# Optimization experiments

Hardware: AMD Instinct MI355X
Metric: run time of the kernel (lower is better)

The kernel has to match this reference:

```python
import jax, jax.numpy as jnp
import numpy as np

EMB = 768
HEADS = 8
HEAD_DIM = EMB // HEADS
SCALE = HEAD_DIM ** -0.5


def setup_inputs() -> dict:
    key = jax.random.key(0)
    ks = jax.random.split(key, 9)
    s = 0.02
    return {
        "x": jax.random.normal(ks[0], (2, 4096, EMB), dtype=jnp.float32),
        "Wq": jax.random.normal(ks[1], (EMB, EMB), dtype=jnp.float32) * s,
        "bq": jax.random.normal(ks[2], (EMB,), dtype=jnp.float32) * s,
        "Wk": jax.random.normal(ks[3], (EMB, EMB), dtype=jnp.float32) * s,
        "bk": jax.random.normal(ks[4], (EMB,), dtype=jnp.float32) * s,
        "Wv": jax.random.normal(ks[5], (EMB, EMB), dtype=jnp.float32) * s,
        "bv": jax.random.normal(ks[6], (EMB,), dtype=jnp.float32) * s,
        "Wo": jax.random.normal(ks[7], (EMB, EMB), dtype=jnp.float32) * s,
        "bo": jax.random.normal(ks[8], (EMB,), dtype=jnp.float32) * s,
    }


def reference(x, Wq, bq, Wk, bk, Wv, bv, Wo, bo):
    b, n, _ = x.shape
    # torch Linear: y = x @ W.T + b
    def split_heads(y):  # [b, n, emb] -> [b, h, n, d]
        return y.reshape(b, n, HEADS, HEAD_DIM).transpose(0, 2, 1, 3)

    q = split_heads(x @ Wq.T + bq)
    k = split_heads(x @ Wk.T + bk)
    v = split_heads(x @ Wv.T + bv)
    # scores [b, h, q, k]; source applies scaling inside softmax input
    scores = jnp.einsum('bhqd,bhkd->bhqk', q, k) * SCALE
    weight = jax.nn.softmax(scores, axis=-1)
    out = jnp.einsum('bhqk,bhkd->bhqd', weight, v)
    out = out.transpose(0, 2, 1, 3).reshape(b, n, EMB)
    return out @ Wo.T + bo
```

## Files before the change

kernel.cpp:

```cpp
#include <hip/hip_runtime.h>


typedef __bf16 bf16;
typedef __attribute__((ext_vector_type(4))) float f32x4;
typedef __attribute__((ext_vector_type(16))) float f32x16;
typedef __attribute__((ext_vector_type(8))) __bf16 bf16x8;
typedef __attribute__((ext_vector_type(4))) __bf16 bf16x4;
typedef __attribute__((ext_vector_type(4))) unsigned u32x4;

#define EMB 768
#define SEQ 4096
#define NB 2
#define NHEADS 8
#define HD 96
#define BHTOT (NB * NHEADS)
#define MTOT (NB * SEQ)
#define QSCALE 0.14724241052735512f

#define AS1 __attribute__((address_space(1)))
#define AS3 __attribute__((address_space(3)))

__global__ __launch_bounds__(256) void cast_f32_bf16(const float* __restrict__ in,
                                                     bf16* __restrict__ out) {
  const int i = (blockIdx.x * 256 + threadIdx.x) * 4;
  const f32x4 v = *reinterpret_cast<const f32x4*>(in + i);
  bf16x4 o;
  o[0] = (bf16)v[0]; o[1] = (bf16)v[1]; o[2] = (bf16)v[2]; o[3] = (bf16)v[3];
  *reinterpret_cast<bf16x4*>(out + i) = o;
}

__global__ __launch_bounds__(256) void cast_w4(const float* __restrict__ w0,
                                               const float* __restrict__ w1,
                                               const float* __restrict__ w2,
                                               const float* __restrict__ w3,
                                               bf16* __restrict__ o0,
                                               bf16* __restrict__ o1,
                                               bf16* __restrict__ o2,
                                               bf16* __restrict__ o3) {
  const float* w = (blockIdx.y == 0) ? w0 : (blockIdx.y == 1) ? w1 : (blockIdx.y == 2) ? w2 : w3;
  bf16* o = (blockIdx.y == 0) ? o0 : (blockIdx.y == 1) ? o1 : (blockIdx.y == 2) ? o2 : o3;
  const int i = (blockIdx.x * 256 + threadIdx.x) * 4;
  const f32x4 v = *reinterpret_cast<const f32x4*>(w + i);
  bf16x4 ob;
  ob[0] = (bf16)v[0]; ob[1] = (bf16)v[1]; ob[2] = (bf16)v[2]; ob[3] = (bf16)v[3];
  *reinterpret_cast<bf16x4*>(o + i) = ob;
}

template <int MODE>
__global__ __launch_bounds__(256) void gemm_bt(const bf16* __restrict__ A,
                                               const bf16* __restrict__ B,
                                               const float* __restrict__ b0,
                                               const float* __restrict__ b1,
                                               const float* __restrict__ b2,
                                               void* __restrict__ out,
                                               void* __restrict__ outK) {
  constexpr int K = EMB;
  __shared__ bf16 As[128 * 32];
  __shared__ bf16 Bs[128 * 32];
  const int tid = threadIdx.x;
  const int lane = tid & 63;
  const int wid = tid >> 6;
  const int wr = wid >> 1, wc = wid & 1;
  const int l15 = lane & 15, l4 = lane >> 4;
  const int rowBase = blockIdx.y * 128;
  const int colBase = blockIdx.x * 128;

  f32x4 acc[4][4] = {};

  for (int kt = 0; kt < K / 32; ++kt) {
    const int kb = kt * 32;
#pragma unroll
    for (int i = 0; i < 2; ++i) {
      const int c = (wid * 2 + i) * 64 + lane;
      const int row = c >> 2, cc = c & 3;
      const bf16* ga = A + (size_t)(rowBase + row) * K + kb + cc * 8;
      const bf16* gb = B + (size_t)(colBase + row) * K + kb + cc * 8;
      __builtin_amdgcn_global_load_lds(
          (const AS1 void*)ga,
          (AS3 void*)(As + (size_t)(wid * 2 + i) * 512), 16, 0, 0);
      __builtin_amdgcn_global_load_lds(
          (const AS1 void*)gb,
          (AS3 void*)(Bs + (size_t)(wid * 2 + i) * 512), 16, 0, 0);
    }
    __syncthreads();
    bf16x8 af[4], bfr[4];
#pragma unroll
    for (int t = 0; t < 4; ++t) {
      af[t]  = *reinterpret_cast<const bf16x8*>(As + (wr * 64 + t * 16 + l15) * 32 + l4 * 8);
      bfr[t] = *reinterpret_cast<const bf16x8*>(Bs + (wc * 64 + t * 16 + l15) * 32 + l4 * 8);
    }
#pragma unroll
    for (int mt = 0; mt < 4; ++mt)
#pragma unroll
      for (int nt = 0; nt < 4; ++nt)
        acc[mt][nt] = __builtin_amdgcn_mfma_f32_16x16x32_bf16(af[mt], bfr[nt], acc[mt][nt], 0, 0, 0);
    __syncthreads();
  }

#pragma unroll
  for (int mt = 0; mt < 4; ++mt) {
#pragma unroll
    for (int nt = 0; nt < 4; ++nt) {
      const int gn = colBase + wc * 64 + nt * 16 + l15;
      if (MODE == 0) {
        const int mm = gn / 768;
        const int g7 = gn - mm * 768;
        const int h = g7 / HD, d = g7 - h * HD;
        const float* bp = (mm == 0) ? b0 : (mm == 1) ? b1 : b2;
        const float bv = bp[g7];
        const float sc = (mm == 0) ? QSCALE : 1.f;
#pragma unroll
        for (int r = 0; r < 4; ++r) {
          const int gm = rowBase + wr * 64 + mt * 16 + l4 * 4 + r;
          const int b = gm >> 12, n = gm & (SEQ - 1);
          const float v = (acc[mt][nt][r] + bv) * sc;
          if (mm == 1) {
            ((bf16*)outK)[((size_t)(b * NHEADS + h) * SEQ + n) * 128 +
                          (((d >> 3) ^ (n & 7)) << 3) + (d & 7)] = (bf16)v;
          } else {
            bf16* dst = (bf16*)out + (mm == 2 ? (size_t)MTOT * EMB : 0);
            dst[((size_t)(b * NHEADS + h) * SEQ + n) * HD + d] = (bf16)v;
          }
        }
      } else {
        const float bv = b0[gn];
#pragma unroll
        for (int r = 0; r < 4; ++r) {
          const int gm = rowBase + wr * 64 + mt * 16 + l4 * 4 + r;
          ((float*)out)[(size_t)gm * EMB + gn] = acc[mt][nt][r] + bv;
        }
      }
    }
  }
}

__global__ __launch_bounds__(256) void transpose_v(const bf16* __restrict__ v,
                                                   bf16* __restrict__ vt) {
  __shared__ bf16 T[96][72];
  const int bh = blockIdx.y;
  const int n0 = blockIdx.x * 64;
  const int tid = threadIdx.x;
#pragma unroll
  for (int i = 0; i < 3; ++i) {
    const int c = i * 256 + tid;
    const int n = c / 12, cc = c % 12;
    const bf16x8 val = *reinterpret_cast<const bf16x8*>(
        v + ((size_t)bh * SEQ + n0 + n) * HD + cc * 8);
#pragma unroll
    for (int j = 0; j < 8; ++j) T[cc * 8 + j][n] = val[j];
  }
  __syncthreads();
#pragma unroll
  for (int i = 0; i < 3; ++i) {
    const int c = i * 256 + tid;
    const int d = c >> 3, nc = c & 7;
    const int s0i = (nc >> 1) * 16 + (nc & 1) * 4;
    const bf16x4 lo = *reinterpret_cast<const bf16x4*>(&T[d][s0i]);
    const bf16x4 hi = *reinterpret_cast<const bf16x4*>(&T[d][s0i + 8]);
    const bf16x8 val = __builtin_shufflevector(lo, hi, 0, 1, 2, 3, 4, 5, 6, 7);
    const int pc = nc ^ (d & 7);
    *reinterpret_cast<bf16x8*>(vt + ((size_t)bh * HD + d) * SEQ + n0 + pc * 8) = val;
  }
}

__global__ __launch_bounds__(256) void attn_fwd(const bf16* __restrict__ q,
                                                const bf16* __restrict__ ksw,
                                                const bf16* __restrict__ vt,
                                                bf16* __restrict__ o) {
  __shared__ bf16 Ks[2][64 * 128];
  __shared__ bf16 Vts[2][96 * 64];
  const int tid = threadIdx.x;
  const int lane = tid & 63;
  const int wid = tid >> 6;
  const int l31 = lane & 31, lhi = lane >> 5;
  const int lin = blockIdx.y * 16 + blockIdx.x;
  const int l2 = (lin & 7) * 32 + (lin >> 3);
  const int qblk = l2 & 15, bh = l2 >> 4;
  const int q0 = qblk * 256 + wid * 64;
  const size_t headq = (size_t)bh * SEQ * HD;
  const bf16* kg = ksw + (size_t)bh * SEQ * 128;
  const bf16* vg = vt + (size_t)bh * (size_t)HD * SEQ;

  const bf16* kp = kg + (size_t)tid * 8;
  const bf16* vp = vg + (size_t)(tid >> 3) * SEQ + (tid & 7) * 8;

  int krd[12], vrd[12];
#pragma unroll
  for (int kib = 0; kib < 2; ++kib)
#pragma unroll
    for (int dc = 0; dc < 6; ++dc) {
      const int row = kib * 32 + l31;
      krd[kib * 6 + dc] = (row * 128 + (((dc * 2 + lhi) ^ (l31 & 7)) * 8)) * 2;
    }
#pragma unroll
  for (int db = 0; db < 3; ++db)
#pragma unroll
    for (int kb = 0; kb < 4; ++kb) {
      const int row = db * 32 + l31;
      vrd[db * 4 + kb] = (row * 64 + (((kb * 2 + lhi) ^ (l31 & 7)) * 8)) * 2;
    }

  bf16x8 qf[2][6];
#pragma unroll
  for (int g = 0; g < 2; ++g)
#pragma unroll
    for (int dc = 0; dc < 6; ++dc)
      qf[g][dc] = *reinterpret_cast<const bf16x8*>(
          q + headq + (size_t)(q0 + g * 32 + l31) * HD + dc * 16 + lhi * 8);

  f32x16 oacc[2][3] = {};
  float lrun[2] = {0.f, 0.f};

#pragma unroll
  for (int i = 0; i < 4; ++i)
    __builtin_amdgcn_global_load_lds((const AS1 void*)(kp + i * 2048),
                                     (AS3 void*)(&Ks[0][i * 2048 + wid * 512]), 16, 0, 0);
#pragma unroll
  for (int i = 0; i < 3; ++i)
    __builtin_amdgcn_global_load_lds((const AS1 void*)(vp + (size_t)i * 131072),
                                     (AS3 void*)(&Vts[0][i * 2048 + wid * 512]), 16, 0, 0);
  kp += 8192;
  vp += 64;
  __syncthreads();

  constexpr int NT = SEQ / 64;
  for (int kt = 0; kt < NT; ++kt) {
    const int cur = kt & 1;
    if (kt < NT - 1) {
#pragma unroll
      for (int i = 0; i < 4; ++i)
        __builtin_amdgcn_global_load_lds((const AS1 void*)(kp + i * 2048),
                                         (AS3 void*)(&Ks[cur ^ 1][i * 2048 + wid * 512]), 16, 0, 0);
#pragma unroll
      for (int i = 0; i < 3; ++i)
        __builtin_amdgcn_global_load_lds((const AS1 void*)(vp + (size_t)i * 131072),
                                         (AS3 void*)(&Vts[cur ^ 1][i * 2048 + wid * 512]), 16, 0, 0);
      kp += 8192;
      vp += 64;
    }
    const char* ksb = (const char*)Ks[cur];
    const char* vsb = (const char*)Vts[cur];

    bf16x8 pf[2][4];
#pragma unroll
    for (int kib = 0; kib < 2; ++kib) {
      f32x16 s[2] = {};
      __builtin_amdgcn_s_setprio(1);
#pragma unroll
      for (int dc = 0; dc < 6; ++dc) {
        const bf16x8 kf = *reinterpret_cast<const bf16x8*>(ksb + krd[kib * 6 + dc]);
        s[0] = __builtin_amdgcn_mfma_f32_32x32x16_bf16(kf, qf[0][dc], s[0], 0, 0, 0);
        s[1] = __builtin_amdgcn_mfma_f32_32x32x16_bf16(kf, qf[1][dc], s[1], 0, 0, 0);
      }
      __builtin_amdgcn_s_setprio(0);
#pragma unroll
      for (int g = 0; g < 2; ++g) {
        float a0 = 0.f, a1 = 0.f, a2 = 0.f, a3 = 0.f;
#pragma unroll
        for (int i = 0; i < 4; ++i) {
          s[g][4 * i + 0] = __builtin_amdgcn_exp2f(s[g][4 * i + 0]); a0 += s[g][4 * i + 0];
          s[g][4 * i + 1] = __builtin_amdgcn_exp2f(s[g][4 * i + 1]); a1 += s[g][4 * i + 1];
          s[g][4 * i + 2] = __builtin_amdgcn_exp2f(s[g][4 * i + 2]); a2 += s[g][4 * i + 2];
          s[g][4 * i + 3] = __builtin_amdgcn_exp2f(s[g][4 * i + 3]); a3 += s[g][4 * i + 3];
        }
        lrun[g] += (a0 + a1) + (a2 + a3);
        unsigned c[8];
#pragma unroll
        for (int i = 0; i < 8; ++i)
          asm("v_cvt_pk_bf16_f32 %0, %1, %2"
              : "=v"(c[i]) : "v"(s[g][2 * i]), "v"(s[g][2 * i + 1]));
        const u32x4 wa = {c[0], c[1], c[2], c[3]};
        const u32x4 wb = {c[4], c[5], c[6], c[7]};
        pf[g][kib * 2 + 0] = __builtin_bit_cast(bf16x8, wa);
        pf[g][kib * 2 + 1] = __builtin_bit_cast(bf16x8, wb);
      }
    }

    __builtin_amdgcn_s_setprio(1);
#pragma unroll
    for (int kb = 0; kb < 4; ++kb) {
#pragma unroll
      for (int db = 0; db < 3; ++db) {
        const bf16x8 vf = *reinterpret_cast<const bf16x8*>(vsb + vrd[db * 4 + kb]);
        oacc[0][db] = __builtin_amdgcn_mfma_f32_32x32x16_bf16(vf, pf[0][kb], oacc[0][db], 0, 0, 0);
        oacc[1][db] = __builtin_amdgcn_mfma_f32_32x32x16_bf16(vf, pf[1][kb], oacc[1][db], 0, 0, 0);
      }
    }
    __builtin_amdgcn_s_setprio(0);

    __syncthreads();
  }

  const int b = bh >> 3, h = bh & 7;
#pragma unroll
  for (int g = 0; g < 2; ++g) {
    float lr = lrun[g];
    lr += __shfl_xor(lr, 32, 64);
    const float inv = 1.f / lr;
    const int n = q0 + g * 32 + l31;
    bf16* obase = o + (size_t)(b * SEQ + n) * EMB + h * HD;
#pragma unroll
    for (int db = 0; db < 3; ++db) {
#pragma unroll
      for (int i = 0; i < 8; ++i) {
        const int r = 2 * i;
        const int d = db * 32 + (r & 3) + 8 * (r >> 2) + 4 * lhi;
        unsigned w;
        const float v0 = oacc[g][db][r] * inv, v1 = oacc[g][db][r + 1] * inv;
        asm("v_cvt_pk_bf16_f32 %0, %1, %2" : "=v"(w) : "v"(v0), "v"(v1));
        *reinterpret_cast<unsigned*>(obase + d) = w;
      }
    }
  }
}

extern "C" void kernel_launch(void* const* d_in, const int* in_sizes, int n_in,
                              void* d_out, int out_size, void* d_ws, size_t ws_size,
                              hipStream_t stream) {
  const float* x  = (const float*)d_in[0];
  const float* Wq = (const float*)d_in[1];
  const float* bq = (const float*)d_in[2];
  const float* Wk = (const float*)d_in[3];
  const float* bk = (const float*)d_in[4];
  const float* Wv = (const float*)d_in[5];
  const float* bv = (const float*)d_in[6];
  const float* Wo = (const float*)d_in[7];
  const float* bo = (const float*)d_in[8];

  const size_t XN = (size_t)MTOT * EMB;
  const size_t WN = (size_t)EMB * EMB;
  const size_t KSWN = (size_t)BHTOT * SEQ * 128;

  bf16* p = (bf16*)d_ws;
  bf16* xbf  = p; p += XN;
  bf16* wqb  = p; p += WN;
  bf16* wkb  = p; p += WN;
  bf16* wvb  = p; p += WN;
  bf16* wob  = p; p += WN;
  bf16* qb   = p; p += XN;
  bf16* vb   = p; p += XN;
  bf16* kbsw = p; p += KSWN;
  bf16* vtb  = p; p += XN;
  bf16* ao   = p; p += XN;

  cast_f32_bf16<<<XN / 1024, 256, 0, stream>>>(x, xbf);
  cast_w4<<<dim3(WN / 1024, 4), 256, 0, stream>>>(Wq, Wk, Wv, Wo, wqb, wkb, wvb, wob);

  gemm_bt<0><<<dim3(3 * EMB / 128, MTOT / 128), 256, 0, stream>>>(
      xbf, wqb, bq, bk, bv, qb, kbsw);

  transpose_v<<<dim3(SEQ / 64, BHTOT), 256, 0, stream>>>(vb, vtb);

  attn_fwd<<<dim3(SEQ / 256, BHTOT), 256, 0, stream>>>(qb, kbsw, vtb, ao);

  gemm_bt<1><<<dim3(EMB / 128, MTOT / 128), 256, 0, stream>>>(
      ao, wob, bo, nullptr, nullptr, d_out, nullptr);
}
```

Before: 237.3 us.

## Split attention KV range in two with fp32 partials and a merge kernel

```diff
diff --git a/kernel.cpp b/kernel.cpp
--- a/kernel.cpp
+++ b/kernel.cpp
@@ -2,6 +2,7 @@
 
 
 typedef __bf16 bf16;
+typedef __attribute__((ext_vector_type(2))) float f32x2;
 typedef __attribute__((ext_vector_type(4))) float f32x4;
 typedef __attribute__((ext_vector_type(16))) float f32x16;
 typedef __attribute__((ext_vector_type(8))) __bf16 bf16x8;
@@ -163,26 +164,34 @@
   }
 }
 
-__global__ __launch_bounds__(256) void attn_fwd(const bf16* __restrict__ q,
-                                                const bf16* __restrict__ ksw,
-                                                const bf16* __restrict__ vt,
-                                                bf16* __restrict__ o) {
+template <int SPLIT>
+__global__ __launch_bounds__(256, 2) void attn_fwd(const bf16* __restrict__ q,
+                                                   const bf16* __restrict__ ksw,
+                                                   const bf16* __restrict__ vt,
+                                                   void* __restrict__ outp,
+                                                   float* __restrict__ lsum) {
   __shared__ bf16 Ks[2][64 * 128];
   __shared__ bf16 Vts[2][96 * 64];
   const int tid = threadIdx.x;
   const int lane = tid & 63;
   const int wid = tid >> 6;
   const int l31 = lane & 31, lhi = lane >> 5;
-  const int lin = blockIdx.y * 16 + blockIdx.x;
-  const int l2 = (lin & 7) * 32 + (lin >> 3);
-  const int qblk = l2 & 15, bh = l2 >> 4;
+  const int lin = (blockIdx.z * gridDim.y + blockIdx.y) * gridDim.x + blockIdx.x;
+  const int nblk = 256 * SPLIT;
+  const int cpx = nblk >> 3;
+  const int l2 = (lin & 7) * cpx + (lin >> 3);
+  const int qblk = l2 & 15;
+  const int z = (SPLIT == 2) ? ((l2 >> 4) & 1) : 0;
+  const int bh = (SPLIT == 2) ? (l2 >> 5) : (l2 >> 4);
   const int q0 = qblk * 256 + wid * 64;
+  constexpr int NT = SEQ / 64 / SPLIT;
+  const int kv00 = z * NT * 64;
   const size_t headq = (size_t)bh * SEQ * HD;
   const bf16* kg = ksw + (size_t)bh * SEQ * 128;
   const bf16* vg = vt + (size_t)bh * (size_t)HD * SEQ;
 
-  const bf16* kp = kg + (size_t)tid * 8;
-  const bf16* vp = vg + (size_t)(tid >> 3) * SEQ + (tid & 7) * 8;
+  const bf16* kp = kg + (size_t)kv00 * 128 + (size_t)tid * 8;
+  const bf16* vp = vg + (size_t)(tid >> 3) * SEQ + kv00 + (tid & 7) * 8;
 
   int krd[12], vrd[12];
 #pragma unroll
@@ -214,27 +223,26 @@
 #pragma unroll
   for (int i = 0; i < 4; ++i)
     __builtin_amdgcn_global_load_lds((const AS1 void*)(kp + i * 2048),
-                                     (AS3 void*)(&Ks[0][i * 2048 + wid * 512]), 16, 0, 0);
+                                     (AS3 void*)(&Ks[0][i * 2048 + tid * 8]), 16, 0, 0);
 #pragma unroll
   for (int i = 0; i < 3; ++i)
-    __builtin_amdgcn_global_load_lds((const AS1 void*)(vp + (size_t)i * 131072),
-                                     (AS3 void*)(&Vts[0][i * 2048 + wid * 512]), 16, 0, 0);
+    __builtin_amdgcn_global_load_lds((const AS1 void*)(vp + (size_t)i * 32 * SEQ),
+                                     (AS3 void*)(&Vts[0][i * 2048 + tid * 8]), 16, 0, 0);
   kp += 8192;
   vp += 64;
   __syncthreads();
 
-  constexpr int NT = SEQ / 64;
   for (int kt = 0; kt < NT; ++kt) {
     const int cur = kt & 1;
     if (kt < NT - 1) {
 #pragma unroll
       for (int i = 0; i < 4; ++i)
         __builtin_amdgcn_global_load_lds((const AS1 void*)(kp + i * 2048),
-                                         (AS3 void*)(&Ks[cur ^ 1][i * 2048 + wid * 512]), 16, 0, 0);
+                                         (AS3 void*)(&Ks[cur ^ 1][i * 2048 + tid * 8]), 16, 0, 0);
 #pragma unroll
       for (int i = 0; i < 3; ++i)
-        __builtin_amdgcn_global_load_lds((const AS1 void*)(vp + (size_t)i * 131072),
-                                         (AS3 void*)(&Vts[cur ^ 1][i * 2048 + wid * 512]), 16, 0, 0);
+        __builtin_amdgcn_global_load_lds((const AS1 void*)(vp + (size_t)i * 32 * SEQ),
+                                         (AS3 void*)(&Vts[cur ^ 1][i * 2048 + tid * 8]), 16, 0, 0);
       kp += 8192;
       vp += 64;
     }
@@ -296,22 +304,54 @@
   for (int g = 0; g < 2; ++g) {
     float lr = lrun[g];
     lr += __shfl_xor(lr, 32, 64);
-    const float inv = 1.f / lr;
     const int n = q0 + g * 32 + l31;
-    bf16* obase = o + (size_t)(b * SEQ + n) * EMB + h * HD;
-#pragma unroll
-    for (int db = 0; db < 3; ++db) {
-#pragma unroll
-      for (int i = 0; i < 8; ++i) {
-        const int r = 2 * i;
-        const int d = db * 32 + (r & 3) + 8 * (r >> 2) + 4 * lhi;
-        unsigned w;
-        const float v0 = oacc[g][db][r] * inv, v1 = oacc[g][db][r + 1] * inv;
-        asm("v_cvt_pk_bf16_f32 %0, %1, %2" : "=v"(w) : "v"(v0), "v"(v1));
-        *reinterpret_cast<unsigned*>(obase + d) = w;
-      }
-    }
-  }
+    if (SPLIT == 2) {
+      float* po = (float*)outp + (size_t)z * ((size_t)BHTOT * SEQ * HD) +
+                  ((size_t)bh * SEQ + n) * HD;
+#pragma unroll
+      for (int db = 0; db < 3; ++db)
+#pragma unroll
+        for (int i = 0; i < 8; ++i) {
+          const int r = 2 * i;
+          const int d = db * 32 + (r & 3) + 8 * (r >> 2) + 4 * lhi;
+          f32x2 w = {oacc[g][db][r], oacc[g][db][r + 1]};
+          *reinterpret_cast<f32x2*>(po + d) = w;
+        }
+      if (lhi == 0) lsum[(size_t)z * BHTOT * SEQ + (size_t)bh * SEQ + n] = lr;
+    } else {
+      const float inv = 1.f / lr;
+      bf16* obase = (bf16*)outp + (size_t)(b * SEQ + n) * EMB + h * HD;
+#pragma unroll
+      for (int db = 0; db < 3; ++db)
+#pragma unroll
+        for (int i = 0; i < 8; ++i) {
+          const int r = 2 * i;
+          const int d = db * 32 + (r & 3) + 8 * (r >> 2) + 4 * lhi;
+          unsigned w;
+          const float v0 = oacc[g][db][r] * inv, v1 = oacc[g][db][r + 1] * inv;
+          asm("v_cvt_pk_bf16_f32 %0, %1, %2" : "=v"(w) : "v"(v0), "v"(v1));
+          *reinterpret_cast<unsigned*>(obase + d) = w;
+        }
+    }
+  }
+}
+
+__global__ __launch_bounds__(256) void merge_o(const float* __restrict__ p,
+                                               const float* __restrict__ ls,
+                                               bf16* __restrict__ ao) {
+  const int idx = blockIdx.x * 256 + threadIdx.x;
+  const size_t PS = (size_t)BHTOT * SEQ * HD;
+  const f32x4 a = *reinterpret_cast<const f32x4*>(p + (size_t)idx * 4);
+  const f32x4 b2 = *reinterpret_cast<const f32x4*>(p + PS + (size_t)idx * 4);
+  const int rest = idx / 24;
+  const int d4 = idx - rest * 24;
+  const float inv = 1.f / (ls[rest] + ls[BHTOT * SEQ + rest]);
+  const int bh = rest >> 12, n = rest & (SEQ - 1);
+  const int b = bh >> 3, h = bh & 7;
+  bf16x4 o4;
+#pragma unroll
+  for (int j = 0; j < 4; ++j) o4[j] = (bf16)((a[j] + b2[j]) * inv);
+  *reinterpret_cast<bf16x4*>(ao + (size_t)(b * SEQ + n) * EMB + h * HD + d4 * 4) = o4;
 }
 
 extern "C" void kernel_launch(void* const* d_in, const int* in_sizes, int n_in,
@@ -342,6 +382,12 @@
   bf16* kbsw = p; p += KSWN;
   bf16* vtb  = p; p += XN;
   bf16* ao   = p; p += XN;
+  const size_t base_bytes = (size_t)((char*)p - (char*)d_ws);
+  float* part = (float*)p;
+  float* lsum = part + 2 * ((size_t)BHTOT * SEQ * HD);
+  const size_t need2 = base_bytes + (2 * (size_t)BHTOT * SEQ * HD) * 4 +
+                       (2 * (size_t)BHTOT * SEQ) * 4;
+  const bool split2 = (ws_size >= need2);
 
   cast_f32_bf16<<<XN / 1024, 256, 0, stream>>>(x, xbf);
   cast_w4<<<dim3(WN / 1024, 4), 256, 0, stream>>>(Wq, Wk, Wv, Wo, wqb, wkb, wvb, wob);
@@ -351,7 +397,12 @@
 
   transpose_v<<<dim3(SEQ / 64, BHTOT), 256, 0, stream>>>(vb, vtb);
 
-  attn_fwd<<<dim3(SEQ / 256, BHTOT), 256, 0, stream>>>(qb, kbsw, vtb, ao);
+  if (split2) {
+    attn_fwd<2><<<dim3(16, 16, 2), 256, 0, stream>>>(qb, kbsw, vtb, part, lsum);
+    merge_o<<<(BHTOT * SEQ * HD / 4) / 256, 256, 0, stream>>>(part, lsum, ao);
+  } else {
+    attn_fwd<1><<<dim3(16, 16, 1), 256, 0, stream>>>(qb, kbsw, vtb, ao, nullptr);
+  }
 
   gemm_bt<1><<<dim3(EMB / 128, MTOT / 128), 256, 0, stream>>>(
       ao, wob, bo, nullptr, nullptr, d_out, nullptr);
```

Measured after the change: 211.0 us. -11.1%, faster.
